# Optimization experiments

Measured on AMD Instinct MI355X. Metric: run time of the kernel, lower is better.

The kernel has to match this reference:

```python
import jax, jax.numpy as jnp
import numpy as np

SINKHORN_ITERS = 50  # fixed iteration count (original uses err-tolerance while-loop)


def sinkhorn(M, a, b, lam):
    # M: [T, V] cost; a: [T, B] topic marginals; b: [V, B] word marginals
    K = jnp.exp(-M * lam)            # [T, V]
    u0 = jnp.ones_like(a) / a.shape[0]

    def step(u, _):
        v = b / (K.T @ u)            # [V, B]
        u = a / (K @ v)              # [T, B]
        return u, None

    u, _ = jax.lax.scan(step, u0, None, length=SINKHORN_ITERS)
    v = b / (K.T @ u)
    # per-document sinkhorn divergence: sum_t u_t * ((K*M) @ v)_t -> [B]
    return jnp.sum(u * ((K * M) @ v), axis=0)


def setup_inputs() -> dict:
    key = jax.random.key(0)
    kx, kt, kw, km, ke = jax.random.split(key, 5)
    B, T, V, E = 2048, 100, 20000, 256
    x = jax.random.uniform(kx, (B, V), dtype=jnp.float32)  # BoW-like weights
    doc_topic = jax.random.uniform(kt, (B, T), dtype=jnp.float32) + 1e-3
    doc_topic = doc_topic / jnp.sum(doc_topic, axis=1, keepdims=True)
    doc_word = jax.random.uniform(kw, (B, V), dtype=jnp.float32) + 1e-3
    doc_word = doc_word / jnp.sum(doc_word, axis=1, keepdims=True)
    M = jax.random.uniform(km, (T, V), dtype=jnp.float32)  # nonneg cost in [0,1)
    topic_embedding = jax.random.normal(ke, (T, E), dtype=jnp.float32)
    return {"x": x, "doc_topic": doc_topic, "doc_word": doc_word, "M": M,
            "topic_embedding": topic_embedding, "sh_alpha": 20,
            "rec_loss_weight": 100}


def reference(x, doc_topic, doc_word, M, topic_embedding, sh_alpha, rec_loss_weight):
    sh_loss = sinkhorn(M, doc_topic.T, doc_word.T, sh_alpha).mean()
    rec_log_probs = jax.nn.log_softmax(doc_topic @ (1.0 - M), axis=1)  # [B, V]
    rec_loss = -jnp.mean(jnp.sum(rec_log_probs * x, axis=1))
    joint_loss = rec_loss_weight * rec_loss + sh_loss
    return (rec_loss, sh_loss, joint_loss)
```

## Files before the change

kernel.cpp:

```cpp
#include <hip/hip_runtime.h>
#include <math.h>

#define B_   2048
#define T_   100
#define V_   20000
#define VP   20480
#define KP   128
#define TP   112
#define NC2  32
#define CH2  640
#define LDV  72

typedef short s8v __attribute__((ext_vector_type(8)));
typedef short s4v __attribute__((ext_vector_type(4)));
typedef float f4  __attribute__((ext_vector_type(4)));

__device__ __forceinline__ short f2bf(float f) {
    unsigned u = __builtin_bit_cast(unsigned, f);
    u += 0x7fffu + ((u >> 16) & 1u);
    return (short)(u >> 16);
}
__device__ __forceinline__ float bf2f(short h) {
    unsigned u = ((unsigned)(unsigned short)h) << 16;
    return __builtin_bit_cast(float, u);
}
#define MFMA(a,b,c) __builtin_amdgcn_mfma_f32_16x16x32_bf16((a),(b),(c),0,0,0)

__global__ void k_initKT(const float* __restrict__ M, const int* __restrict__ alpha,
                         short* __restrict__ A1, short* __restrict__ W1) {
    __shared__ float tile[32][33];
    float lam = (float)(*alpha);
    int v0 = blockIdx.x * 32, t0 = blockIdx.y * 32;
    int tx = threadIdx.x, ty = threadIdx.y;
    for (int j = 0; j < 4; ++j) {
        int t = t0 + ty + 8 * j, v = v0 + tx;
        tile[ty + 8 * j][tx] = (t < T_ && v < V_) ? M[(size_t)t * V_ + v] : 0.f;
    }
    __syncthreads();
    for (int j = 0; j < 4; ++j) {
        int t = t0 + tx, v = v0 + ty + 8 * j;
        float m = tile[tx][ty + 8 * j];
        bool valid = (t < T_) && (v < V_);
        A1[(size_t)v * KP + t] = valid ? f2bf(__expf(-m * lam)) : (short)0;
        W1[(size_t)v * KP + t] = valid ? f2bf(1.f - m) : (short)0;
    }
}

__global__ void k_initA2(const float* __restrict__ M, const int* __restrict__ alpha,
                         short* __restrict__ A2, short* __restrict__ A2M) {
    float lam = (float)(*alpha);
    size_t id = (size_t)blockIdx.x * 256 + threadIdx.x;
    int t = (int)(id / VP), v = (int)(id % VP);
    bool valid = (t < T_) && (v < V_);
    float m = valid ? M[(size_t)t * V_ + v] : 0.f;
    float k = valid ? __expf(-m * lam) : 0.f;
    A2[id]  = valid ? f2bf(k) : (short)0;
    A2M[id] = valid ? f2bf(k * m) : (short)0;
}

__global__ void k_init0(short* __restrict__ uTbf, float* __restrict__ recSE,
                        float* __restrict__ recSXL, float* __restrict__ recSX) {
    int id = blockIdx.x * 256 + threadIdx.x;
    int t = id & (KP - 1);
    uTbf[id] = (t < T_) ? f2bf(0.01f) : (short)0;
    if (id < B_) { recSE[id] = 0.f; recSXL[id] = 0.f; recSX[id] = 0.f; }
}

__global__ void k_castdw(const float* __restrict__ dw, short* __restrict__ dwbf) {
    size_t base = ((size_t)blockIdx.x * 256 + threadIdx.x) * 8;
    f4 x0 = *(const f4*)(dw + base);
    f4 x1 = *(const f4*)(dw + base + 4);
    s8v o;
    o[0]=f2bf(x0[0]); o[1]=f2bf(x0[1]); o[2]=f2bf(x0[2]); o[3]=f2bf(x0[3]);
    o[4]=f2bf(x1[0]); o[5]=f2bf(x1[1]); o[6]=f2bf(x1[2]); o[7]=f2bf(x1[3]);
    *(s8v*)(dwbf + base) = o;
}

__global__ void k_castdt(const float* __restrict__ dt, short* __restrict__ dtbf) {
    int id = blockIdx.x * 256 + threadIdx.x;
    int b = id >> 7, t = id & (KP - 1);
    dtbf[id] = (t < T_) ? f2bf(dt[(size_t)b * T_ + t]) : (short)0;
}

__global__ __launch_bounds__(256, 2) void k_GF(const short* __restrict__ A1,
                                               const short* __restrict__ A2acc,
                                               const short* __restrict__ uT,
                                               const short* __restrict__ dwbf,
                                               float* __restrict__ part2) {
    __shared__ short vv[4][32 * LDV];
    int tid = threadIdx.x;
    int wave = tid >> 6, lane = tid & 63, q = lane >> 4, l16 = lane & 15;

    int l = blockIdx.x;
    int j = l & 31, bx = l >> 5;
    int c = ((j & 7) << 2) | (j >> 3);
    int v0 = c * CH2;
    int b0 = bx * 128 + wave * 32;
    short* buf = vv[wave];

    s8v au[2][4];
#pragma unroll
    for (int cb = 0; cb < 2; ++cb)
#pragma unroll
        for (int ks = 0; ks < 4; ++ks)
            au[cb][ks] = *(const s8v*)(uT + (size_t)(b0 + cb * 16 + l16) * KP + ks * 32 + q * 8);

    f4 acc2[7][2];
#pragma unroll
    for (int tt = 0; tt < 7; ++tt) { acc2[tt][0] = (f4)0.f; acc2[tt][1] = (f4)0.f; }

    for (int s = 0; s < 10; ++s) {
        int vs = v0 + s * 64;
        s4v dwv[2][4];
#pragma unroll
        for (int cb = 0; cb < 2; ++cb)
#pragma unroll
            for (int vt = 0; vt < 4; ++vt) {
                int vg = vs + vt * 16 + q * 4;
                dwv[cb][vt] = (vg < V_)
                    ? *(const s4v*)(dwbf + (size_t)(b0 + cb * 16 + l16) * V_ + vg)
                    : (s4v)0;
            }
        f4 acc1[2][4];
#pragma unroll
        for (int cb = 0; cb < 2; ++cb)
#pragma unroll
            for (int vt = 0; vt < 4; ++vt) acc1[cb][vt] = (f4)0.f;
#pragma unroll
        for (int ks = 0; ks < 4; ++ks) {
            int ko = ks * 32 + q * 8;
            s8v bv[4];
#pragma unroll
            for (int vt = 0; vt < 4; ++vt)
                bv[vt] = *(const s8v*)(A1 + (size_t)(vs + vt * 16 + l16) * KP + ko);
#pragma unroll
            for (int cb = 0; cb < 2; ++cb)
#pragma unroll
                for (int vt = 0; vt < 4; ++vt)
                    acc1[cb][vt] = MFMA(bv[vt], au[cb][ks], acc1[cb][vt]);
        }
#pragma unroll
        for (int cb = 0; cb < 2; ++cb)
#pragma unroll
            for (int vt = 0; vt < 4; ++vt) {
                int vg = vs + vt * 16 + q * 4;
                s4v o;
                if (vg < V_) {
#pragma unroll
                    for (int r = 0; r < 4; ++r)
                        o[r] = f2bf(bf2f(dwv[cb][vt][r]) * __builtin_amdgcn_rcpf(acc1[cb][vt][r]));
                } else {
                    o = (s4v)0;
                }
                *(s4v*)(buf + (cb * 16 + l16) * LDV + vt * 16 + q * 4) = o;
            }
        asm volatile("s_waitcnt lgkmcnt(0)" ::: "memory");
        __builtin_amdgcn_sched_barrier(0);
#pragma unroll
        for (int ks2 = 0; ks2 < 2; ++ks2) {
            int ko = ks2 * 32 + q * 8;
            s8v bb[2];
#pragma unroll
            for (int cb = 0; cb < 2; ++cb)
                bb[cb] = *(const s8v*)(buf + (cb * 16 + l16) * LDV + ko);
#pragma unroll
            for (int tt = 0; tt < 7; ++tt) {
                s8v a = *(const s8v*)(A2acc + (size_t)(tt * 16 + l16) * VP + vs + ko);
#pragma unroll
                for (int cb = 0; cb < 2; ++cb)
                    acc2[tt][cb] = MFMA(a, bb[cb], acc2[tt][cb]);
            }
        }
        __builtin_amdgcn_s_barrier();
    }
#pragma unroll
    for (int tt = 0; tt < 7; ++tt)
#pragma unroll
        for (int cb = 0; cb < 2; ++cb) {
            int bg = b0 + cb * 16 + l16;
            *(f4*)(part2 + ((size_t)c * B_ + bg) * TP + tt * 16 + q * 4) = acc2[tt][cb];
        }
}

__global__ void k_R(const float* __restrict__ part2, const float* __restrict__ dt,
                    float* __restrict__ uf, short* __restrict__ uTbf,
                    float* __restrict__ kmvf, int mode) {
    int id = blockIdx.x * 256 + threadIdx.x;
    int b = id / 28, t4 = (id % 28) * 4;
    f4 s = (f4)0.f;
    for (int c = 0; c < NC2; ++c)
        s += *(const f4*)(part2 + ((size_t)c * B_ + b) * TP + t4);
    if (mode == 0) {
#pragma unroll
        for (int j = 0; j < 4; ++j) {
            int t = t4 + j;
            float v = (t < T_) ? dt[(size_t)b * T_ + t] / s[j] : 0.f;
            uf[(size_t)b * TP + t] = v;
            uTbf[(size_t)b * KP + t] = f2bf(v);
        }
    } else {
#pragma unroll
        for (int j = 0; j < 4; ++j) kmvf[(size_t)b * TP + t4 + j] = s[j];
    }
}

__global__ __launch_bounds__(256, 2) void k_rec(const short* __restrict__ dtbf,
                                                const short* __restrict__ W1,
                                                const float* __restrict__ x,
                                                float* __restrict__ recSE,
                                                float* __restrict__ recSXL,
                                                float* __restrict__ recSX) {
    __shared__ float lg[64 * 260];
    int tid = threadIdx.x;
    int wave = tid >> 6, lane = tid & 63, q = lane >> 4, l16 = lane & 15;
    int v0 = blockIdx.x * 256;
    int b0 = blockIdx.y * 64;
    int bw = b0 + wave * 16;
    f4 acc[16];
#pragma unroll
    for (int vt = 0; vt < 16; ++vt) acc[vt] = (f4)0.f;
#pragma unroll
    for (int ks = 0; ks < 4; ++ks) {
        int ko = ks * 32 + q * 8;
        s8v a = *(const s8v*)(dtbf + (size_t)(bw + l16) * KP + ko);
#pragma unroll
        for (int vt = 0; vt < 16; ++vt) {
            s8v bb = *(const s8v*)(W1 + (size_t)(v0 + vt * 16 + l16) * KP + ko);
            acc[vt] = MFMA(a, bb, acc[vt]);
        }
    }
#pragma unroll
    for (int vt = 0; vt < 16; ++vt)
#pragma unroll
        for (int r = 0; r < 4; ++r)
            lg[(wave * 16 + q * 4 + r) * 260 + vt * 16 + l16] = acc[vt][r];
    __syncthreads();
    int bl = tid >> 2, seg = tid & 3;
    int bg = b0 + bl;
    float se = 0.f, sxl = 0.f, sx = 0.f;
#pragma unroll
    for (int i = 0; i < 16; ++i) {
        int vl = seg * 64 + i * 4;
        int vg = v0 + vl;
        f4 lo = *(f4*)(&lg[bl * 260 + vl]);
        if (vg + 3 < V_) {
            f4 xv = *(const f4*)(x + (size_t)bg * V_ + vg);
#pragma unroll
            for (int j = 0; j < 4; ++j) {
                se += __expf(lo[j]); sxl += lo[j] * xv[j]; sx += xv[j];
            }
        } else {
#pragma unroll
            for (int j = 0; j < 4; ++j)
                if (vg + j < V_) {
                    float xv = x[(size_t)bg * V_ + vg + j];
                    se += __expf(lo[j]); sxl += lo[j] * xv; sx += xv;
                }
        }
    }
    se  += __shfl_xor(se, 1, 64);  se  += __shfl_xor(se, 2, 64);
    sxl += __shfl_xor(sxl, 1, 64); sxl += __shfl_xor(sxl, 2, 64);
    sx  += __shfl_xor(sx, 1, 64);  sx  += __shfl_xor(sx, 2, 64);
    if (seg == 0) {
        atomicAdd(&recSE[bg], se);
        atomicAdd(&recSXL[bg], sxl);
        atomicAdd(&recSX[bg], sx);
    }
}

__global__ void k_div(const float* __restrict__ uf, const float* __restrict__ kmvf,
                      float* __restrict__ divb) {
    int b = blockIdx.x * 256 + threadIdx.x;
    if (b >= B_) return;
    float s = 0.f;
    for (int t = 0; t < TP; ++t) s += uf[(size_t)b * TP + t] * kmvf[(size_t)b * TP + t];
    divb[b] = s;
}

__global__ void k_final(const float* __restrict__ divb, const float* __restrict__ recSE,
                        const float* __restrict__ recSXL, const float* __restrict__ recSX,
                        const int* __restrict__ wptr, float* __restrict__ out) {
    __shared__ float sA[256], sB[256];
    int tid = threadIdx.x;
    float accS = 0.f, accR = 0.f;
    for (int b = tid; b < B_; b += 256) {
        accS += divb[b];
        accR += recSXL[b] - logf(recSE[b]) * recSX[b];
    }
    sA[tid] = accS; sB[tid] = accR;
    __syncthreads();
    for (int s = 128; s > 0; s >>= 1) {
        if (tid < s) { sA[tid] += sA[tid + s]; sB[tid] += sB[tid + s]; }
        __syncthreads();
    }
    if (tid == 0) {
        float sh = sA[0] / (float)B_;
        float rec = -sB[0] / (float)B_;
        out[0] = rec;
        out[1] = sh;
        out[2] = (float)(*wptr) * rec + sh;
    }
}

extern "C" void kernel_launch(void* const* d_in, const int* in_sizes, int n_in,
                              void* d_out, int out_size, void* d_ws, size_t ws_size,
                              hipStream_t stream) {
    const float* x  = (const float*)d_in[0];
    const float* dt = (const float*)d_in[1];
    const float* dw = (const float*)d_in[2];
    const float* M  = (const float*)d_in[3];
    const int* alpha = (const int*)d_in[5];
    const int* wrec  = (const int*)d_in[6];
    float* out = (float*)d_out;

    char* p = (char*)d_ws;
    short* A1   = (short*)p; p += (size_t)VP * KP * 2;
    short* W1   = (short*)p; p += (size_t)VP * KP * 2;
    short* A2   = (short*)p; p += (size_t)TP * VP * 2;
    short* A2M  = (short*)p; p += (size_t)TP * VP * 2;
    short* uTbf = (short*)p; p += (size_t)B_ * KP * 2;
    short* dtbf = (short*)p; p += (size_t)B_ * KP * 2;
    short* dwbf = (short*)p; p += (size_t)B_ * V_ * 2;
    float* part2 = (float*)p; p += (size_t)NC2 * B_ * TP * 4;
    float* uf    = (float*)p; p += (size_t)B_ * TP * 4;
    float* kmvf  = (float*)p; p += (size_t)B_ * TP * 4;
    float* recSE  = (float*)p; p += B_ * 4;
    float* recSXL = (float*)p; p += B_ * 4;
    float* recSX  = (float*)p; p += B_ * 4;
    float* divb   = (float*)p; p += B_ * 4;

    k_initKT<<<dim3(VP / 32, 4), dim3(32, 8), 0, stream>>>(M, alpha, A1, W1);
    k_initA2<<<(TP * VP) / 256, 256, 0, stream>>>(M, alpha, A2, A2M);
    k_init0<<<(B_ * KP) / 256, 256, 0, stream>>>(uTbf, recSE, recSXL, recSX);
    k_castdw<<<(B_ * V_) / (256 * 8), 256, 0, stream>>>(dw, dwbf);
    k_castdt<<<(B_ * KP) / 256, 256, 0, stream>>>(dt, dtbf);
    k_rec<<<dim3(79, B_ / 64), 256, 0, stream>>>(dtbf, W1, x, recSE, recSXL, recSX);

    for (int it = 0; it < 50; ++it) {
        k_GF<<<dim3((B_ / 128) * NC2), 256, 0, stream>>>(A1, A2, uTbf, dwbf, part2);
        k_R<<<(B_ * 28) / 256, 256, 0, stream>>>(part2, dt, uf, uTbf, kmvf, 0);
    }
    k_GF<<<dim3((B_ / 128) * NC2), 256, 0, stream>>>(A1, A2M, uTbf, dwbf, part2);
    k_R<<<(B_ * 28) / 256, 256, 0, stream>>>(part2, dt, uf, uTbf, kmvf, 1);
    k_div<<<B_ / 256, 256, 0, stream>>>(uf, kmvf, divb);
    k_final<<<1, 256, 0, stream>>>(divb, recSE, recSXL, recSX, wrec, out);
}
```

Baseline: 5.110 ms.

## Prefetch A2 fragments in Sinkhorn kernel and drop LDS staging in rec kernel

```diff
diff --git a/kernel.cpp b/kernel.cpp
--- a/kernel.cpp
+++ b/kernel.cpp
@@ -121,6 +121,13 @@
                     ? *(const s4v*)(dwbf + (size_t)(b0 + cb * 16 + l16) * V_ + vg)
                     : (s4v)0;
             }
+        s8v a2r[2][7];
+#pragma unroll
+        for (int ks2 = 0; ks2 < 2; ++ks2)
+#pragma unroll
+            for (int tt = 0; tt < 7; ++tt)
+                a2r[ks2][tt] = *(const s8v*)(A2acc + (size_t)(tt * 16 + l16) * VP
+                                             + vs + ks2 * 32 + q * 8);
         f4 acc1[2][4];
 #pragma unroll
         for (int cb = 0; cb < 2; ++cb)
@@ -154,8 +161,6 @@
                 }
                 *(s4v*)(buf + (cb * 16 + l16) * LDV + vt * 16 + q * 4) = o;
             }
-        asm volatile("s_waitcnt lgkmcnt(0)" ::: "memory");
-        __builtin_amdgcn_sched_barrier(0);
 #pragma unroll
         for (int ks2 = 0; ks2 < 2; ++ks2) {
             int ko = ks2 * 32 + q * 8;
@@ -164,12 +169,10 @@
             for (int cb = 0; cb < 2; ++cb)
                 bb[cb] = *(const s8v*)(buf + (cb * 16 + l16) * LDV + ko);
 #pragma unroll
-            for (int tt = 0; tt < 7; ++tt) {
-                s8v a = *(const s8v*)(A2acc + (size_t)(tt * 16 + l16) * VP + vs + ko);
+            for (int tt = 0; tt < 7; ++tt)
 #pragma unroll
                 for (int cb = 0; cb < 2; ++cb)
-                    acc2[tt][cb] = MFMA(a, bb[cb], acc2[tt][cb]);
-            }
+                    acc2[tt][cb] = MFMA(a2r[ks2][tt], bb[cb], acc2[tt][cb]);
         }
         __builtin_amdgcn_s_barrier();
     }
@@ -204,64 +207,50 @@
     }
 }
 
-__global__ __launch_bounds__(256, 2) void k_rec(const short* __restrict__ dtbf,
+__global__ __launch_bounds__(256, 4) void k_rec(const short* __restrict__ dtbf,
                                                 const short* __restrict__ W1,
                                                 const float* __restrict__ x,
                                                 float* __restrict__ recSE,
                                                 float* __restrict__ recSXL,
                                                 float* __restrict__ recSX) {
-    __shared__ float lg[64 * 260];
     int tid = threadIdx.x;
     int wave = tid >> 6, lane = tid & 63, q = lane >> 4, l16 = lane & 15;
     int v0 = blockIdx.x * 256;
     int b0 = blockIdx.y * 64;
-    int bw = b0 + wave * 16;
+    int bg = b0 + wave * 16 + l16;
+    s8v a[4];
+#pragma unroll
+    for (int ks = 0; ks < 4; ++ks)
+        a[ks] = *(const s8v*)(dtbf + (size_t)bg * KP + ks * 32 + q * 8);
     f4 acc[16];
 #pragma unroll
     for (int vt = 0; vt < 16; ++vt) acc[vt] = (f4)0.f;
 #pragma unroll
     for (int ks = 0; ks < 4; ++ks) {
         int ko = ks * 32 + q * 8;
-        s8v a = *(const s8v*)(dtbf + (size_t)(bw + l16) * KP + ko);
 #pragma unroll
         for (int vt = 0; vt < 16; ++vt) {
-            s8v bb = *(const s8v*)(W1 + (size_t)(v0 + vt * 16 + l16) * KP + ko);
-            acc[vt] = MFMA(a, bb, acc[vt]);
-        }
-    }
-#pragma unroll
-    for (int vt = 0; vt < 16; ++vt)
-#pragma unroll
-        for (int r = 0; r < 4; ++r)
-            lg[(wave * 16 + q * 4 + r) * 260 + vt * 16 + l16] = acc[vt][r];
-    __syncthreads();
-    int bl = tid >> 2, seg = tid & 3;
-    int bg = b0 + bl;
+            s8v w = *(const s8v*)(W1 + (size_t)(v0 + vt * 16 + l16) * KP + ko);
+            acc[vt] = MFMA(w, a[ks], acc[vt]);
+        }
+    }
     float se = 0.f, sxl = 0.f, sx = 0.f;
 #pragma unroll
-    for (int i = 0; i < 16; ++i) {
-        int vl = seg * 64 + i * 4;
-        int vg = v0 + vl;
-        f4 lo = *(f4*)(&lg[bl * 260 + vl]);
-        if (vg + 3 < V_) {
+    for (int vt = 0; vt < 16; ++vt) {
+        int vg = v0 + vt * 16 + q * 4;
+        if (vg < V_) {
             f4 xv = *(const f4*)(x + (size_t)bg * V_ + vg);
 #pragma unroll
-            for (int j = 0; j < 4; ++j) {
-                se += __expf(lo[j]); sxl += lo[j] * xv[j]; sx += xv[j];
+            for (int r = 0; r < 4; ++r) {
+                float lo = acc[vt][r];
+                se += __expf(lo); sxl += lo * xv[r]; sx += xv[r];
             }
-        } else {
-#pragma unroll
-            for (int j = 0; j < 4; ++j)
-                if (vg + j < V_) {
-                    float xv = x[(size_t)bg * V_ + vg + j];
-                    se += __expf(lo[j]); sxl += lo[j] * xv; sx += xv;
-                }
-        }
-    }
-    se  += __shfl_xor(se, 1, 64);  se  += __shfl_xor(se, 2, 64);
-    sxl += __shfl_xor(sxl, 1, 64); sxl += __shfl_xor(sxl, 2, 64);
-    sx  += __shfl_xor(sx, 1, 64);  sx  += __shfl_xor(sx, 2, 64);
-    if (seg == 0) {
+        }
+    }
+    se  += __shfl_xor(se, 16, 64);  se  += __shfl_xor(se, 32, 64);
+    sxl += __shfl_xor(sxl, 16, 64); sxl += __shfl_xor(sxl, 32, 64);
+    sx  += __shfl_xor(sx, 16, 64);  sx  += __shfl_xor(sx, 32, 64);
+    if (q == 0) {
         atomicAdd(&recSE[bg], se);
         atomicAdd(&recSXL[bg], sxl);
         atomicAdd(&recSX[bg], sx);
```

Measured after the change: 4.992 ms. 2.3% less time.
